# Kernel tuning notes

Hardware: AMD Instinct MI355X
Metric: run time of the kernel (lower is better)

## Reference

```python
import jax, jax.numpy as jnp
import numpy as np

G = 4            # groups
IN_G = 16        # input_dim // groups
OUT_G = 32       # output_dim // groups
DEG = 3          # legendre degree
K = 3            # kernel size
EPS = 1e-5       # InstanceNorm eps


def _conv(x, w):
    # NCHW x OIHW, stride 1, padding 1 (SAME-like for k=3)
    return jax.lax.conv_general_dilated(
        x, w, window_strides=(1, 1), padding=((1, 1), (1, 1)),
        dimension_numbers=('NCHW', 'OIHW', 'NCHW'))


def setup_inputs() -> dict:
    key = jax.random.key(0)
    kx, kb, kp = jax.random.split(key, 3)
    x = jax.random.normal(kx, (32, 64, 112, 112), dtype=jnp.float32)
    # base conv weights, one per group, kaiming-uniform-ish scale
    fan_b = IN_G * K * K
    base_w = jax.random.uniform(kb, (G, OUT_G, IN_G, K, K), dtype=jnp.float32,
                                minval=-1.0, maxval=1.0) * np.sqrt(3.0 / fan_b)
    fan_p = IN_G * (DEG + 1) * K * K
    poly_w = jax.random.uniform(kp, (G, OUT_G, IN_G * (DEG + 1), K, K), dtype=jnp.float32,
                                minval=-1.0, maxval=1.0) * np.sqrt(3.0 / fan_p)
    return {"x": x, "base_w": base_w, "poly_w": poly_w}


def _legendre_basis(xn, degree):
    # xn: [B, C, H, W] in [-1, 1]; returns [B, C*(degree+1), H, W]
    polys = [jnp.ones_like(xn), xn]
    for n in range(1, degree):
        pn = ((2.0 * n + 1.0) * xn * polys[-1] - n * polys[-2]) / (n + 1.0)
        polys.append(pn)
    return jnp.concatenate(polys, axis=1)


def _forward(x, base_w, poly_w):
    outs = []
    for g in range(G):  # small fixed loop over groups
        xg = x[:, g * IN_G:(g + 1) * IN_G]
        base = _conv(xg, base_w[g])
        mn, mx = jnp.min(xg), jnp.max(xg)
        xn = 2.0 * (xg - mn) / (mx - mn) - 1.0
        basis = _legendre_basis(xn, DEG)            # [B, IN_G*(DEG+1), H, W]
        y = base + _conv(basis, poly_w[g])          # [B, OUT_G, H, W]
        # InstanceNorm2d (affine=False): per-sample, per-channel over spatial
        mu = jnp.mean(y, axis=(2, 3), keepdims=True)
        var = jnp.var(y, axis=(2, 3), keepdims=True)
        yn = (y - mu) * jax.lax.rsqrt(var + EPS)
        outs.append(jax.nn.silu(yn))
    return jnp.concatenate(outs, axis=1)


def reference(x, base_w, poly_w):
    return _forward(x, base_w, poly_w)
```

## Files before the change

kernel.cpp:

```cpp
#include <hip/hip_runtime.h>
#include <hip/hip_bf16.h>

#define HW 112
#define HWHW 12544
#define NB 32
#define CIN 64
#define G 4
#define IN_G 16
#define OUT_G 32
#define NC (NB * G * OUT_G)

typedef _Float16 f16;
typedef _Float16 f16x8 __attribute__((ext_vector_type(8)));
typedef _Float16 f16x4 __attribute__((ext_vector_type(4)));
typedef float f32x4 __attribute__((ext_vector_type(4)));

__device__ __forceinline__ unsigned enc_f32(float f) {
    unsigned u = __float_as_uint(f);
    return (u & 0x80000000u) ? ~u : (u | 0x80000000u);
}
__device__ __forceinline__ float dec_f32(unsigned k) {
    unsigned u = (k & 0x80000000u) ? (k & 0x7fffffffu) : ~k;
    return __uint_as_float(u);
}

__global__ __launch_bounds__(256) void init_kernel(unsigned* __restrict__ mm,
                                                   float* __restrict__ stats) {
    int i = blockIdx.x * 256 + threadIdx.x;
    if (i < 2 * NC) stats[i] = 0.0f;
    if (blockIdx.x == 0 && threadIdx.x < 2 * G)
        mm[threadIdx.x] = (threadIdx.x & 1) ? 0u : 0xFFFFFFFFu;
}

__global__ __launch_bounds__(256) void minmax_kernel(const float* __restrict__ x,
                                                     unsigned* __restrict__ mm) {
    const int pc = blockIdx.x;
    const int g = (pc & 63) >> 4;
    const float* p = x + (size_t)pc * HWHW;
    float lmin = 3.4e38f, lmax = -3.4e38f;
    for (int i = threadIdx.x; i < HWHW / 4; i += 256) {
        float4 v = ((const float4*)p)[i];
        lmin = fminf(lmin, fminf(fminf(v.x, v.y), fminf(v.z, v.w)));
        lmax = fmaxf(lmax, fmaxf(fmaxf(v.x, v.y), fmaxf(v.z, v.w)));
    }
    for (int o = 32; o > 0; o >>= 1) {
        lmin = fminf(lmin, __shfl_down(lmin, o));
        lmax = fmaxf(lmax, __shfl_down(lmax, o));
    }
    __shared__ float smn[4], smx[4];
    int wid = threadIdx.x >> 6, lane = threadIdx.x & 63;
    if (lane == 0) { smn[wid] = lmin; smx[wid] = lmax; }
    __syncthreads();
    if (threadIdx.x == 0) {
        float m0 = fminf(fminf(smn[0], smn[1]), fminf(smn[2], smn[3]));
        float m1 = fmaxf(fmaxf(smx[0], smx[1]), fmaxf(smx[2], smx[3]));
        atomicMin(&mm[2 * g],     enc_f32(m0));
        atomicMax(&mm[2 * g + 1], enc_f32(m1));
    }
}

__global__ __launch_bounds__(256) void fold_kernel(const float* __restrict__ bw,
                                                   const float* __restrict__ pw,
                                                   const unsigned* __restrict__ mm,
                                                   f16* __restrict__ Wf) {
    int idx = blockIdx.x * 256 + threadIdx.x;
    if (idx >= G * OUT_G * IN_G * 9) return;
    int g  = idx / (OUT_G * IN_G * 9);
    int r  = idx - g * (OUT_G * IN_G * 9);
    int co = r / (IN_G * 9);
    int r2 = r - co * (IN_G * 9);
    int ci = r2 / 9, tap = r2 - (r2 / 9) * 9;

    const float mn = dec_f32(mm[2 * g]);
    const float mx = dec_f32(mm[2 * g + 1]);
    const float a = 2.0f / (mx - mn);
    const float b = -a * mn - 1.0f;

    const float bwv = bw[((g * OUT_G + co) * IN_G + ci) * 9 + tap];
    const float* pwb = pw + (size_t)(g * OUT_G + co) * 64 * 9;
    const float p0 = pwb[(0  + ci) * 9 + tap];
    const float p1 = pwb[(16 + ci) * 9 + tap];
    const float p2 = pwb[(32 + ci) * 9 + tap];
    const float p3 = pwb[(48 + ci) * 9 + tap];

    const float W0 = p0 + p1 * b + p2 * (1.5f * b * b - 0.5f) + p3 * (2.5f * b * b * b - 1.5f * b);
    const float W1 = bwv + p1 * a + p2 * (3.0f * a * b) + p3 * (7.5f * a * b * b - 1.5f * a);
    const float W2 = p2 * (1.5f * a * a) + p3 * (7.5f * a * a * b);
    const float W3 = p3 * (2.5f * a * a * a);

    const int h = ci >> 3, cil = ci & 7;
    f16x4 v; v[0] = (f16)W0; v[1] = (f16)W1; v[2] = (f16)W2; v[3] = (f16)W3;
    size_t off = ((size_t)(((g * 2 + h) * 9 + tap) * OUT_G + co)) * 32 + cil * 4;
    *(f16x4*)(Wf + off) = v;
}

__device__ __forceinline__ int swz(int p, int u) {
    return p * 64 + ((u ^ (p & 3) ^ ((p >> 2) & 1)) << 4);
}

__global__ __launch_bounds__(256) void conv_mfma(const float* __restrict__ x,
                                                 const f16* __restrict__ Wf,
                                                 float* __restrict__ out,
                                                 float* __restrict__ stats) {
    const int tile = blockIdx.x, g = blockIdx.y, n = blockIdx.z;
    const int ty0 = (tile / 7) * 16, tx0 = (tile % 7) * 16;

    __shared__ __align__(16) char As[324 * 64];
    __shared__ float sred[2][32];

    const int tid = threadIdx.x;
    const int l = tid & 63, w = tid >> 6;
    const int lx = l & 15, qu = l >> 4;

    if (tid < 64) ((float*)sred)[tid] = 0.0f;

    const float* xg = x + ((size_t)n * CIN + g * IN_G) * HWHW;
    const f16* WfG = Wf + (size_t)g * 2 * 9 * 1024;

    f32x4 acc[4][2];
#pragma unroll
    for (int rr = 0; rr < 4; ++rr)
#pragma unroll
        for (int c = 0; c < 2; ++c) acc[rr][c] = (f32x4)0.0f;

#pragma unroll
    for (int h = 0; h < 2; ++h) {
        f16x8 B[9][2];
#pragma unroll
        for (int t = 0; t < 9; ++t)
#pragma unroll
            for (int c = 0; c < 2; ++c)
                B[t][c] = *(const f16x8*)(WfG + ((size_t)((h * 9 + t) * 32 + c * 16 + lx)) * 32 + qu * 8);

        for (int it = 0; it < 6; ++it) {
            int j = tid + it * 256;
            if (j < 1296) {
                int cip = j / 324, p = j - cip * 324;
                int py = p / 18, px_ = p - py * 18;
                int gy = ty0 + py - 1, gx = tx0 + px_ - 1;
                bool ok = (gy >= 0) & (gy < HW) & (gx >= 0) & (gx < HW);
                const float* src = xg + (size_t)(h * 8 + 2 * cip) * HWHW + gy * HW + gx;
                float v0 = ok ? src[0] : 0.0f;
                float v1 = ok ? src[HWHW] : 0.0f;
                f16 one = ok ? (f16)1.0f : (f16)0.0f;
                f16x8 pk;
                pk[0] = one; pk[1] = (f16)v0; pk[2] = (f16)(v0 * v0); pk[3] = (f16)(v0 * v0 * v0);
                pk[4] = one; pk[5] = (f16)v1; pk[6] = (f16)(v1 * v1); pk[7] = (f16)(v1 * v1 * v1);
                *(f16x8*)(&As[swz(p, cip)]) = pk;
            }
        }
        __syncthreads();

#pragma unroll
        for (int kw = 0; kw < 3; ++kw) {
            f16x8 a[6];
#pragma unroll
            for (int r = 0; r < 6; ++r) {
                int pl = (4 * w + r) * 18 + lx + kw;
                a[r] = *(const f16x8*)(&As[swz(pl, qu)]);
            }
#pragma unroll
            for (int r = 0; r < 6; ++r)
#pragma unroll
                for (int kh = 0; kh < 3; ++kh) {
                    const int rr = r - kh;
                    if (rr >= 0 && rr < 4) {
                        acc[rr][0] = __builtin_amdgcn_mfma_f32_16x16x32_f16(a[r], B[kh * 3 + kw][0], acc[rr][0], 0, 0, 0);
                        acc[rr][1] = __builtin_amdgcn_mfma_f32_16x16x32_f16(a[r], B[kh * 3 + kw][1], acc[rr][1], 0, 0, 0);
                    }
                }
        }
        __syncthreads();
    }

    float s0 = 0.f, ss0 = 0.f, s1 = 0.f, ss1 = 0.f;
#pragma unroll
    for (int rr = 0; rr < 4; ++rr)
#pragma unroll
        for (int j = 0; j < 4; ++j) {
            float v0 = acc[rr][0][j], v1 = acc[rr][1][j];
            s0 += v0; ss0 += v0 * v0;
            s1 += v1; ss1 += v1 * v1;
        }
    s0 += __shfl_xor(s0, 16); ss0 += __shfl_xor(ss0, 16);
    s0 += __shfl_xor(s0, 32); ss0 += __shfl_xor(ss0, 32);
    s1 += __shfl_xor(s1, 16); ss1 += __shfl_xor(ss1, 16);
    s1 += __shfl_xor(s1, 32); ss1 += __shfl_xor(ss1, 32);
    if (qu == 0) {
        atomicAdd(&sred[0][lx],      s0); atomicAdd(&sred[1][lx],      ss0);
        atomicAdd(&sred[0][16 + lx], s1); atomicAdd(&sred[1][16 + lx], ss1);
    }

    const size_t ob = ((size_t)n * (G * OUT_G) + g * OUT_G) * HWHW;
#pragma unroll
    for (int rr = 0; rr < 4; ++rr) {
        const int y = ty0 + 4 * w + rr;
#pragma unroll
        for (int c = 0; c < 2; ++c) {
            float* dst = out + ob + (size_t)(c * 16 + lx) * HWHW + (size_t)y * HW + tx0 + qu * 4;
            *(f32x4*)dst = acc[rr][c];
        }
    }

    __syncthreads();
    if (tid < 32) {
        const size_t slot = (size_t)n * (G * OUT_G) + g * OUT_G + tid;
        atomicAdd(&stats[slot * 2],     sred[0][tid]);
        atomicAdd(&stats[slot * 2 + 1], sred[1][tid]);
    }
}

__global__ __launch_bounds__(256) void apply_kernel(float* __restrict__ out,
                                                    const float* __restrict__ stats) {
    const int nc = blockIdx.x;
    const float s  = stats[nc * 2];
    const float ss = stats[nc * 2 + 1];
    const float mu = s * (1.0f / HWHW);
    const float rs = rsqrtf(ss * (1.0f / HWHW) - mu * mu + 1e-5f);
    float* p = out + (size_t)nc * HWHW;
    for (int i = threadIdx.x; i < HWHW / 4; i += 256) {
        float4 v = ((const float4*)p)[i];
        v.x = (v.x - mu) * rs; v.x = v.x / (1.0f + __expf(-v.x));
        v.y = (v.y - mu) * rs; v.y = v.y / (1.0f + __expf(-v.y));
        v.z = (v.z - mu) * rs; v.z = v.z / (1.0f + __expf(-v.z));
        v.w = (v.w - mu) * rs; v.w = v.w / (1.0f + __expf(-v.w));
        ((float4*)p)[i] = v;
    }
}

extern "C" void kernel_launch(void* const* d_in, const int* in_sizes, int n_in,
                              void* d_out, int out_size, void* d_ws, size_t ws_size,
                              hipStream_t stream) {
    const float* x  = (const float*)d_in[0];
    const float* bw = (const float*)d_in[1];
    const float* pw = (const float*)d_in[2];
    float* out = (float*)d_out;

    unsigned* mm = (unsigned*)d_ws;
    float* stats = (float*)((char*)d_ws + 1024);
    f16* Wf = (f16*)((char*)d_ws + 34816);

    init_kernel<<<32, 256, 0, stream>>>(mm, stats);
    minmax_kernel<<<NB * CIN, 256, 0, stream>>>(x, mm);
    fold_kernel<<<144, 256, 0, stream>>>(bw, pw, mm, Wf);
    conv_mfma<<<dim3(49, G, NB), 256, 0, stream>>>(x, Wf, out, stats);
    apply_kernel<<<NC, 256, 0, stream>>>(out, stats);
}
```

Measured before the change: 522.4 us.

## Stage both channel halves in LDS once and stream weights per kw

The conv kernel now fills a doubled LDS tile holding all 16 input channels' Legendre power features in a single pass, with an XOR swizzle keyed on column. This removes the per-half barrier pairs. Weight fragments are loaded from global per kw (3 taps at a time) instead of holding all 18 in registers, and launch bounds request 3 blocks per SM to raise occupancy. The shared-memory stats reduction is replaced by direct global atomics from each wave, which removes a barrier but raises global atomic traffic fourfold. The larger LDS footprint (about 41 KB) may limit how many blocks fit per CU.

```diff
diff --git a/kernel.cpp b/kernel.cpp
--- a/kernel.cpp
+++ b/kernel.cpp
@@ -94,28 +94,40 @@
     *(f16x4*)(Wf + off) = v;
 }
 
-__device__ __forceinline__ int swz(int p, int u) {
-    return p * 64 + ((u ^ (p & 3) ^ ((p >> 2) & 1)) << 4);
-}
-
-__global__ __launch_bounds__(256) void conv_mfma(const float* __restrict__ x,
-                                                 const f16* __restrict__ Wf,
-                                                 float* __restrict__ out,
-                                                 float* __restrict__ stats) {
+__global__ __launch_bounds__(256, 3) void conv_mfma(const float* __restrict__ x,
+                                                    const f16* __restrict__ Wf,
+                                                    float* __restrict__ out,
+                                                    float* __restrict__ stats) {
     const int tile = blockIdx.x, g = blockIdx.y, n = blockIdx.z;
     const int ty0 = (tile / 7) * 16, tx0 = (tile % 7) * 16;
 
-    __shared__ __align__(16) char As[324 * 64];
-    __shared__ float sred[2][32];
+    __shared__ __align__(16) char As[324 * 128];
 
     const int tid = threadIdx.x;
     const int l = tid & 63, w = tid >> 6;
     const int lx = l & 15, qu = l >> 4;
 
-    if (tid < 64) ((float*)sred)[tid] = 0.0f;
-
     const float* xg = x + ((size_t)n * CIN + g * IN_G) * HWHW;
     const f16* WfG = Wf + (size_t)g * 2 * 9 * 1024;
+    const f16* Wlane = WfG + lx * 32 + qu * 8;
+
+    for (int it = 0; it < 11; ++it) {
+        int j = tid + it * 256;
+        if (j < 2592) {
+            int cip = j / 324, p = j - cip * 324;
+            int py = p / 18, px_ = p - py * 18;
+            int gy = ty0 + py - 1, gx = tx0 + px_ - 1;
+            bool ok = (gy >= 0) & (gy < HW) & (gx >= 0) & (gx < HW);
+            const float* src = xg + (size_t)(2 * cip) * HWHW + gy * HW + gx;
+            float v0 = ok ? src[0] : 0.0f;
+            float v1 = ok ? src[HWHW] : 0.0f;
+            f16 one = ok ? (f16)1.0f : (f16)0.0f;
+            f16x8 pk;
+            pk[0] = one; pk[1] = (f16)v0; pk[2] = (f16)(v0 * v0); pk[3] = (f16)(v0 * v0 * v0);
+            pk[4] = one; pk[5] = (f16)v1; pk[6] = (f16)(v1 * v1); pk[7] = (f16)(v1 * v1 * v1);
+            *(f16x8*)(&As[p * 128 + ((cip ^ (px_ & 7)) << 4)]) = pk;
+        }
+    }
 
     f32x4 acc[4][2];
 #pragma unroll
@@ -123,41 +135,26 @@
 #pragma unroll
         for (int c = 0; c < 2; ++c) acc[rr][c] = (f32x4)0.0f;
 
+    __syncthreads();
+
 #pragma unroll
     for (int h = 0; h < 2; ++h) {
-        f16x8 B[9][2];
-#pragma unroll
-        for (int t = 0; t < 9; ++t)
-#pragma unroll
-            for (int c = 0; c < 2; ++c)
-                B[t][c] = *(const f16x8*)(WfG + ((size_t)((h * 9 + t) * 32 + c * 16 + lx)) * 32 + qu * 8);
-
-        for (int it = 0; it < 6; ++it) {
-            int j = tid + it * 256;
-            if (j < 1296) {
-                int cip = j / 324, p = j - cip * 324;
-                int py = p / 18, px_ = p - py * 18;
-                int gy = ty0 + py - 1, gx = tx0 + px_ - 1;
-                bool ok = (gy >= 0) & (gy < HW) & (gx >= 0) & (gx < HW);
-                const float* src = xg + (size_t)(h * 8 + 2 * cip) * HWHW + gy * HW + gx;
-                float v0 = ok ? src[0] : 0.0f;
-                float v1 = ok ? src[HWHW] : 0.0f;
-                f16 one = ok ? (f16)1.0f : (f16)0.0f;
-                f16x8 pk;
-                pk[0] = one; pk[1] = (f16)v0; pk[2] = (f16)(v0 * v0); pk[3] = (f16)(v0 * v0 * v0);
-                pk[4] = one; pk[5] = (f16)v1; pk[6] = (f16)(v1 * v1); pk[7] = (f16)(v1 * v1 * v1);
-                *(f16x8*)(&As[swz(p, cip)]) = pk;
+#pragma unroll
+        for (int kw = 0; kw < 3; ++kw) {
+            f16x8 B0[3], B1[3];
+#pragma unroll
+            for (int kh = 0; kh < 3; ++kh) {
+                const f16* bp = Wlane + (size_t)(h * 9 + kh * 3 + kw) * 1024;
+                B0[kh] = *(const f16x8*)bp;
+                B1[kh] = *(const f16x8*)(bp + 512);
             }
-        }
-        __syncthreads();
-
-#pragma unroll
-        for (int kw = 0; kw < 3; ++kw) {
+            const int col = lx + kw;
+            const int ubase = ((qu + 4 * h) ^ (col & 7)) << 4;
             f16x8 a[6];
 #pragma unroll
             for (int r = 0; r < 6; ++r) {
-                int pl = (4 * w + r) * 18 + lx + kw;
-                a[r] = *(const f16x8*)(&As[swz(pl, qu)]);
+                int pl = (4 * w + r) * 18 + col;
+                a[r] = *(const f16x8*)(&As[pl * 128 + ubase]);
             }
 #pragma unroll
             for (int r = 0; r < 6; ++r)
@@ -165,12 +162,11 @@
                 for (int kh = 0; kh < 3; ++kh) {
                     const int rr = r - kh;
                     if (rr >= 0 && rr < 4) {
-                        acc[rr][0] = __builtin_amdgcn_mfma_f32_16x16x32_f16(a[r], B[kh * 3 + kw][0], acc[rr][0], 0, 0, 0);
-                        acc[rr][1] = __builtin_amdgcn_mfma_f32_16x16x32_f16(a[r], B[kh * 3 + kw][1], acc[rr][1], 0, 0, 0);
+                        acc[rr][0] = __builtin_amdgcn_mfma_f32_16x16x32_f16(a[r], B0[kh], acc[rr][0], 0, 0, 0);
+                        acc[rr][1] = __builtin_amdgcn_mfma_f32_16x16x32_f16(a[r], B1[kh], acc[rr][1], 0, 0, 0);
                     }
                 }
         }
-        __syncthreads();
     }
 
     float s0 = 0.f, ss0 = 0.f, s1 = 0.f, ss1 = 0.f;
@@ -187,8 +183,11 @@
     s1 += __shfl_xor(s1, 16); ss1 += __shfl_xor(ss1, 16);
     s1 += __shfl_xor(s1, 32); ss1 += __shfl_xor(ss1, 32);
     if (qu == 0) {
-        atomicAdd(&sred[0][lx],      s0); atomicAdd(&sred[1][lx],      ss0);
-        atomicAdd(&sred[0][16 + lx], s1); atomicAdd(&sred[1][16 + lx], ss1);
+        const size_t slot = (size_t)n * (G * OUT_G) + g * OUT_G + lx;
+        atomicAdd(&stats[slot * 2],            s0);
+        atomicAdd(&stats[slot * 2 + 1],        ss0);
+        atomicAdd(&stats[(slot + 16) * 2],     s1);
+        atomicAdd(&stats[(slot + 16) * 2 + 1], ss1);
     }
 
     const size_t ob = ((size_t)n * (G * OUT_G) + g * OUT_G) * HWHW;
@@ -200,13 +199,6 @@
             float* dst = out + ob + (size_t)(c * 16 + lx) * HWHW + (size_t)y * HW + tx0 + qu * 4;
             *(f32x4*)dst = acc[rr][c];
         }
-    }
-
-    __syncthreads();
-    if (tid < 32) {
-        const size_t slot = (size_t)n * (G * OUT_G) + g * OUT_G + tid;
-        atomicAdd(&stats[slot * 2],     sred[0][tid]);
-        atomicAdd(&stats[slot * 2 + 1], sred[1][tid]);
     }
 }
 
```

Result: slower. 541.3 us (+3.6%).
